# Kernel optimization log

Measured on AMD Instinct MI355X. Metric: run time of the kernel, lower is better.

## Reference

```python
import jax, jax.numpy as jnp
import numpy as np
from jax import lax

H = 32  # hidden size (hardcoded in the torch module)

def setup_inputs() -> dict:
    key = jax.random.key(0)
    ks = jax.random.split(key, 7)
    B, T, I = 2048, 512, 64
    s = 1.0 / np.sqrt(H)  # torch nn.LSTM default init scale
    return {
        "x": jax.random.normal(ks[0], (B, T, I), dtype=jnp.float32),
        "W_ih": jax.random.uniform(ks[1], (4 * H, I), jnp.float32, -s, s),
        "W_hh": jax.random.uniform(ks[2], (4 * H, H), jnp.float32, -s, s),
        "b_ih": jax.random.uniform(ks[3], (4 * H,), jnp.float32, -s, s),
        "b_hh": jax.random.uniform(ks[4], (4 * H,), jnp.float32, -s, s),
        "W_fc": jax.random.uniform(ks[5], (1, H), jnp.float32, -s, s),
        "b_fc": jax.random.uniform(ks[6], (1,), jnp.float32, -s, s),
    }

def _lstm_last_h(x, W_ih, W_hh, b_ih, b_hh):
    B = x.shape[0]
    # Precompute input projections for all timesteps: [B, T, 4H] -> [T, B, 4H]
    xg = jnp.einsum('bti,gi->btg', x, W_ih) + (b_ih + b_hh)
    xg = jnp.transpose(xg, (1, 0, 2))

    def step(carry, xt):
        h, c = carry
        g = xt + h @ W_hh.T  # [B, 4H]
        i = jax.nn.sigmoid(g[:, 0 * H:1 * H])
        f = jax.nn.sigmoid(g[:, 1 * H:2 * H])
        gg = jnp.tanh(g[:, 2 * H:3 * H])
        o = jax.nn.sigmoid(g[:, 3 * H:4 * H])
        c = f * c + i * gg
        h = o * jnp.tanh(c)
        return (h, c), None

    init = (jnp.zeros((B, H), x.dtype), jnp.zeros((B, H), x.dtype))
    (h, _), _ = lax.scan(step, init, xg)
    return h  # [B, H], last timestep hidden state

def reference(x, W_ih, W_hh, b_ih, b_hh, W_fc, b_fc):
    # Dropout is identity in eval mode; only the last timestep feeds fc.
    h = _lstm_last_h(x, W_ih, W_hh, b_ih, b_hh)
    return h @ W_fc.T + b_fc  # [B, 1]
```

## Files before the change

### kernel.cpp

```cpp
#include <hip/hip_runtime.h>

typedef __attribute__((ext_vector_type(8))) short short8;
typedef __attribute__((ext_vector_type(4))) float f32x4;

#define LOG2E 1.44269504088896340736f

__device__ __forceinline__ unsigned short f2bf(float f) {
    union { float f; unsigned u; } a; a.f = f;
    unsigned r = a.u + 0x7fffu + ((a.u >> 16) & 1u);
    return (unsigned short)(r >> 16);
}
__device__ __forceinline__ unsigned pk2(float x, float y) {
    return (unsigned)f2bf(x) | ((unsigned)f2bf(y) << 16);
}
__device__ __forceinline__ float fsigmoid(float x) {
    return __builtin_amdgcn_rcpf(1.0f + __builtin_amdgcn_exp2f(-LOG2E * x));
}

__global__ __launch_bounds__(256, 2) void lstm_fused(
    const float* __restrict__ x,
    const float* __restrict__ Wih,
    const float* __restrict__ Whh,
    const float* __restrict__ bih,
    const float* __restrict__ bhh,
    const float* __restrict__ Wfc,
    const float* __restrict__ bfc,
    float* __restrict__ out)
{
    __shared__ unsigned short Wlds[128 * 80];
    __shared__ float xg_sh[4 * 16 * 132];
    __shared__ float h_sh[4 * 32];

    const int tid  = threadIdx.x;
    const int lane = tid & 63;
    const int wv   = tid >> 6;
    const int b    = blockIdx.x * 4 + wv;

    {
        const float4* w4 = (const float4*)Wih;
        unsigned* wl = (unsigned*)Wlds;
        #pragma unroll
        for (int i = 0; i < 8; i++) {
            int fi = tid * 8 + i;
            int g  = fi >> 4;
            int k  = (fi & 15) << 2;
            float4 v = w4[fi];
            wl[g * 40 + (k >> 1) + 0] = pk2(v.x, v.y);
            wl[g * 40 + (k >> 1) + 1] = pk2(v.z, v.w);
        }
    }

    float w0[32], w1[32];
    {
        const float4* wh4 = (const float4*)Whh;
        #pragma unroll
        for (int i = 0; i < 8; i++) {
            float4 v = wh4[lane * 8 + i];
            w0[4*i+0] = v.x; w0[4*i+1] = v.y; w0[4*i+2] = v.z; w0[4*i+3] = v.w;
        }
        #pragma unroll
        for (int i = 0; i < 8; i++) {
            float4 v = wh4[(lane + 64) * 8 + i];
            w1[4*i+0] = v.x; w1[4*i+1] = v.y; w1[4*i+2] = v.z; w1[4*i+3] = v.w;
        }
    }
    const float bias0 = bih[lane]      + bhh[lane];
    const float bias1 = bih[lane + 64] + bhh[lane + 64];
    const float kmul  = (lane < 32) ? 2.0f : 1.0f;
    const float ksub  = (lane < 32) ? 1.0f : 0.0f;

    __syncthreads();

    const int m    = lane & 15;
    const int quad = lane >> 4;

    const float* xrow = x + ((size_t)b * 512 + m) * 64;
    float* xgw = xg_sh + wv * 2112;
    float* hw  = h_sh  + wv * 32;

    float hr[32];
    #pragma unroll
    for (int k = 0; k < 32; k++) hr[k] = 0.0f;
    float c = 0.0f, h = 0.0f;

    for (int ch = 0; ch < 32; ++ch) {
        const float4* xr4 = (const float4*)(xrow + ch * 1024);
        float4 l0 = xr4[quad * 2];
        float4 l1 = xr4[quad * 2 + 1];
        float4 l2 = xr4[8 + quad * 2];
        float4 l3 = xr4[8 + quad * 2 + 1];
        union { short8 v; unsigned u[4]; } A0, A1;
        A0.u[0] = pk2(l0.x, l0.y); A0.u[1] = pk2(l0.z, l0.w);
        A0.u[2] = pk2(l1.x, l1.y); A0.u[3] = pk2(l1.z, l1.w);
        A1.u[0] = pk2(l2.x, l2.y); A1.u[1] = pk2(l2.z, l2.w);
        A1.u[2] = pk2(l3.x, l3.y); A1.u[3] = pk2(l3.z, l3.w);

        #pragma unroll
        for (int n = 0; n < 8; n++) {
            const short8 B0 = *(const short8*)&Wlds[(16 * n + m) * 80 + quad * 8];
            const short8 B1 = *(const short8*)&Wlds[(16 * n + m) * 80 + 32 + quad * 8];
            f32x4 acc = {0.f, 0.f, 0.f, 0.f};
            acc = __builtin_amdgcn_mfma_f32_16x16x32_bf16(A0.v, B0, acc, 0, 0, 0);
            acc = __builtin_amdgcn_mfma_f32_16x16x32_bf16(A1.v, B1, acc, 0, 0, 0);
            const int pos = ((n & 3) << 5) + 2 * m + (n >> 2);
            #pragma unroll
            for (int r = 0; r < 4; r++)
                xgw[(quad * 4 + r) * 132 + pos] = acc[r];
        }

        #pragma unroll 2
        for (int tt = 0; tt < 16; ++tt) {
            const float2 xg2 = *(const float2*)&xgw[tt * 132 + 2 * lane];
            float g0 = bias0 + xg2.x;
            float g1 = bias1 + xg2.y;
            #pragma unroll
            for (int k = 0; k < 32; k++) {
                g0 = fmaf(w0[k], hr[k], g0);
                g1 = fmaf(w1[k], hr[k], g1);
            }
            const float s0 = fsigmoid(g0);
            const float v1 = fsigmoid(g1 * kmul);
            const float s1 = fmaf(v1, kmul, -ksub);
            const float f_ = __shfl(s0, lane ^ 32);
            const float o_ = __shfl(s1, lane ^ 32);
            c = fmaf(f_, c, s0 * s1);
            const float th = fmaf(2.0f, fsigmoid(2.0f * c), -1.0f);
            h = o_ * th;
            if (lane < 32) hw[lane] = h;
            #pragma unroll
            for (int i = 0; i < 8; i++) {
                float4 hv = *(const float4*)&hw[i * 4];
                hr[4*i+0] = hv.x; hr[4*i+1] = hv.y; hr[4*i+2] = hv.z; hr[4*i+3] = hv.w;
            }
        }
    }

    float p = (lane < 32) ? h * Wfc[lane & 31] : 0.0f;
    #pragma unroll
    for (int msk = 16; msk >= 1; msk >>= 1) p += __shfl_xor(p, msk);
    if (lane == 0) out[b] = p + bfc[0];
}

extern "C" void kernel_launch(void* const* d_in, const int* in_sizes, int n_in,
                              void* d_out, int out_size, void* d_ws, size_t ws_size,
                              hipStream_t stream) {
    const float* x   = (const float*)d_in[0];
    const float* Wih = (const float*)d_in[1];
    const float* Whh = (const float*)d_in[2];
    const float* bih = (const float*)d_in[3];
    const float* bhh = (const float*)d_in[4];
    const float* Wfc = (const float*)d_in[5];
    const float* bfc = (const float*)d_in[6];
    float* out = (float*)d_out;
    lstm_fused<<<dim3(512), dim3(256), 0, stream>>>(x, Wih, Whh, bih, bhh, Wfc, bfc, out);
}
```

Measured before the change: 490.3 us.

## Compute recurrent h·W_hh via bf16 MFMA instead of scalar FMAs

The per-timestep recurrent matvec (64 scalar FMAs per lane from register-held W_hh) is replaced with eight 16x16x32 bf16 MFMAs. The hidden state is stored in LDS as bf16 and broadcast as the A operand, and the needed outputs are picked with lane selects. The bias is folded into the precomputed input projection, and both half-waves compute the cell state redundantly so h is written by all lanes. This shortens the serial per-step critical path and frees many VGPRs. The cost is bf16 rounding of h and W_hh across 512 recurrent steps, which may compound numerical error, and most of each MFMA's output is wasted.

After: 477.2 us. 2.7% less time.

```diff
diff --git a/kernel.cpp b/kernel.cpp
--- a/kernel.cpp
+++ b/kernel.cpp
@@ -13,9 +13,6 @@
 __device__ __forceinline__ unsigned pk2(float x, float y) {
     return (unsigned)f2bf(x) | ((unsigned)f2bf(y) << 16);
 }
-__device__ __forceinline__ float fsigmoid(float x) {
-    return __builtin_amdgcn_rcpf(1.0f + __builtin_amdgcn_exp2f(-LOG2E * x));
-}
 
 __global__ __launch_bounds__(256, 2) void lstm_fused(
     const float* __restrict__ x,
@@ -29,12 +26,14 @@
 {
     __shared__ unsigned short Wlds[128 * 80];
     __shared__ float xg_sh[4 * 16 * 132];
-    __shared__ float h_sh[4 * 32];
+    __shared__ alignas(64) unsigned short hbuf[4 * 32];
 
     const int tid  = threadIdx.x;
     const int lane = tid & 63;
     const int wv   = tid >> 6;
     const int b    = blockIdx.x * 4 + wv;
+    const int m    = lane & 15;
+    const int quad = lane >> 4;
 
     {
         const float4* w4 = (const float4*)Wih;
@@ -50,38 +49,37 @@
         }
     }
 
-    float w0[32], w1[32];
-    {
-        const float4* wh4 = (const float4*)Whh;
-        #pragma unroll
-        for (int i = 0; i < 8; i++) {
-            float4 v = wh4[lane * 8 + i];
-            w0[4*i+0] = v.x; w0[4*i+1] = v.y; w0[4*i+2] = v.z; w0[4*i+3] = v.w;
-        }
-        #pragma unroll
-        for (int i = 0; i < 8; i++) {
-            float4 v = wh4[(lane + 64) * 8 + i];
-            w1[4*i+0] = v.x; w1[4*i+1] = v.y; w1[4*i+2] = v.z; w1[4*i+3] = v.w;
-        }
+    short8 Bh[8];
+    #pragma unroll
+    for (int t = 0; t < 8; t++) {
+        const float4* wr = (const float4*)(Whh + (size_t)(16 * t + m) * 32 + quad * 8);
+        float4 va = wr[0], vb = wr[1];
+        union { short8 v; unsigned u[4]; } B;
+        B.u[0] = pk2(va.x, va.y); B.u[1] = pk2(va.z, va.w);
+        B.u[2] = pk2(vb.x, vb.y); B.u[3] = pk2(vb.z, vb.w);
+        Bh[t] = B.v;
     }
-    const float bias0 = bih[lane]      + bhh[lane];
-    const float bias1 = bih[lane + 64] + bhh[lane + 64];
-    const float kmul  = (lane < 32) ? 2.0f : 1.0f;
-    const float ksub  = (lane < 32) ? 1.0f : 0.0f;
+
+    float biasv[8];
+    #pragma unroll
+    for (int n = 0; n < 8; n++) biasv[n] = bih[16 * n + m] + bhh[16 * n + m];
+
+    const float kmul = (lane < 32) ? 2.0f : 1.0f;
+    const float ksub = (lane < 32) ? 1.0f : 0.0f;
+    const float kl   = -LOG2E * kmul;
+    const bool  q0   = (lane & 16) != 0;
+    const bool  q1   = (lane & 32) != 0;
+    const bool  lo   = (lane < 32);
 
     __syncthreads();
 
-    const int m    = lane & 15;
-    const int quad = lane >> 4;
-
     const float* xrow = x + ((size_t)b * 512 + m) * 64;
     float* xgw = xg_sh + wv * 2112;
-    float* hw  = h_sh  + wv * 32;
+    unsigned short* hw = hbuf + wv * 32;
 
-    float hr[32];
-    #pragma unroll
-    for (int k = 0; k < 32; k++) hr[k] = 0.0f;
+    hw[lane & 31] = 0;
     float c = 0.0f, h = 0.0f;
+    const f32x4 z4 = {0.f, 0.f, 0.f, 0.f};
 
     for (int ch = 0; ch < 32; ++ch) {
         const float4* xr4 = (const float4*)(xrow + ch * 1024);
@@ -105,37 +103,45 @@
             const int pos = ((n & 3) << 5) + 2 * m + (n >> 2);
             #pragma unroll
             for (int r = 0; r < 4; r++)
-                xgw[(quad * 4 + r) * 132 + pos] = acc[r];
+                xgw[(quad * 4 + r) * 132 + pos] = acc[r] + biasv[n];
         }
 
-        #pragma unroll 2
+        #pragma unroll
         for (int tt = 0; tt < 16; ++tt) {
+            const short8 abf = *(const short8*)&hw[quad * 8];
+            const f32x4 a0 = __builtin_amdgcn_mfma_f32_16x16x32_bf16(abf, Bh[0], z4, 0, 0, 0);
+            const f32x4 a1 = __builtin_amdgcn_mfma_f32_16x16x32_bf16(abf, Bh[1], z4, 0, 0, 0);
+            const f32x4 a2 = __builtin_amdgcn_mfma_f32_16x16x32_bf16(abf, Bh[2], z4, 0, 0, 0);
+            const f32x4 a3 = __builtin_amdgcn_mfma_f32_16x16x32_bf16(abf, Bh[3], z4, 0, 0, 0);
+            const f32x4 a4 = __builtin_amdgcn_mfma_f32_16x16x32_bf16(abf, Bh[4], z4, 0, 0, 0);
+            const f32x4 a5 = __builtin_amdgcn_mfma_f32_16x16x32_bf16(abf, Bh[5], z4, 0, 0, 0);
+            const f32x4 a6 = __builtin_amdgcn_mfma_f32_16x16x32_bf16(abf, Bh[6], z4, 0, 0, 0);
+            const f32x4 a7 = __builtin_amdgcn_mfma_f32_16x16x32_bf16(abf, Bh[7], z4, 0, 0, 0);
+            const float hh0 = q1 ? (q0 ? a3[0] : a2[0]) : (q0 ? a1[0] : a0[0]);
+            const float hh1 = q1 ? (q0 ? a7[0] : a6[0]) : (q0 ? a5[0] : a4[0]);
+
             const float2 xg2 = *(const float2*)&xgw[tt * 132 + 2 * lane];
-            float g0 = bias0 + xg2.x;
-            float g1 = bias1 + xg2.y;
-            #pragma unroll
-            for (int k = 0; k < 32; k++) {
-                g0 = fmaf(w0[k], hr[k], g0);
-                g1 = fmaf(w1[k], hr[k], g1);
-            }
-            const float s0 = fsigmoid(g0);
-            const float v1 = fsigmoid(g1 * kmul);
+            const float g0 = xg2.x + hh0;
+            const float g1 = xg2.y + hh1;
+
+            const float s0 = __builtin_amdgcn_rcpf(1.0f + __builtin_amdgcn_exp2f(-LOG2E * g0));
+            const float v1 = __builtin_amdgcn_rcpf(1.0f + __builtin_amdgcn_exp2f(kl * g1));
             const float s1 = fmaf(v1, kmul, -ksub);
             const float f_ = __shfl(s0, lane ^ 32);
             const float o_ = __shfl(s1, lane ^ 32);
-            c = fmaf(f_, c, s0 * s1);
-            const float th = fmaf(2.0f, fsigmoid(2.0f * c), -1.0f);
-            h = o_ * th;
-            if (lane < 32) hw[lane] = h;
-            #pragma unroll
-            for (int i = 0; i < 8; i++) {
-                float4 hv = *(const float4*)&hw[i * 4];
-                hr[4*i+0] = hv.x; hr[4*i+1] = hv.y; hr[4*i+2] = hv.z; hr[4*i+3] = hv.w;
-            }
+            const float ui = lo ? s0 : f_;
+            const float vg = lo ? s1 : o_;
+            const float wf = lo ? f_ : s0;
+            c = fmaf(wf, c, ui * vg);
+            const float th = fmaf(2.0f, __builtin_amdgcn_rcpf(
+                                 1.0f + __builtin_amdgcn_exp2f(-2.0f * LOG2E * c)), -1.0f);
+            const float oo = lo ? o_ : s1;
+            h = oo * th;
+            hw[lane & 31] = f2bf(h);
         }
     }
 
-    float p = (lane < 32) ? h * Wfc[lane & 31] : 0.0f;
+    float p = lo ? h * Wfc[lane & 31] : 0.0f;
     #pragma unroll
     for (int msk = 16; msk >= 1; msk >>= 1) p += __shfl_xor(p, msk);
     if (lane == 0) out[b] = p + bfc[0];
```
